# Kernel tuning notes

Hardware: AMD Instinct MI355X
Metric: run time of the kernel (lower is better)

## Reference

```python
import jax, jax.numpy as jnp
import numpy as np

N = 131072
C = 8
W = 256


def setup_inputs() -> dict:
    key = jax.random.key(0)
    ks = jax.random.split(key, 10)
    s1 = 1.0 / np.sqrt(3.0)
    sw = 1.0 / np.sqrt(W)
    return {
        "positions": jax.random.normal(ks[0], (N, 3), dtype=jnp.float32),
        "times": jax.random.randint(ks[1], (N,), 0, C, dtype=jnp.int64),
        "W1": jax.random.normal(ks[2], (C, 3, W), dtype=jnp.float32) * s1,
        "b1": jnp.zeros((C, W), dtype=jnp.float32),
        "W2": jax.random.normal(ks[3], (C, W, W), dtype=jnp.float32) * sw,
        "b2": jnp.zeros((C, W), dtype=jnp.float32),
        "W3": jax.random.normal(ks[4], (C, W, W), dtype=jnp.float32) * sw,
        "b3": jnp.zeros((C, W), dtype=jnp.float32),
        "W4": jax.random.normal(ks[5], (C, W, 3), dtype=jnp.float32) * sw,
        "b4": jnp.zeros((C, 3), dtype=jnp.float32),
    }


def _mlp(x, w1, c1, w2, c2, w3, c3, w4, c4):
    # 4-layer MLP, Tanh hidden activations and Tanh output activation
    h = jnp.tanh(x @ w1 + c1)
    h = jnp.tanh(h @ w2 + c2)
    h = jnp.tanh(h @ w3 + c3)
    return jnp.tanh(h @ w4 + c4)


def reference(positions, times, W1, b1, W2, b2, W3, b3, W4, b4):
    # offsets = zeros_like(positions); offsets[times==i] = mlp_i(positions[times==i])
    # classes partition the points, so this equals a per-class select-sum.
    offsets = jnp.zeros_like(positions)
    for i in range(C):  # small fixed class count
        out_i = _mlp(positions, W1[i], b1[i], W2[i], b2[i], W3[i], b3[i], W4[i], b4[i])
        mask = (times == i)[:, None]  # [N,1]
        offsets = jnp.where(mask, out_i, offsets)
    return offsets
```

## Files before the change

### kernel.cpp

```cpp
#include <hip/hip_runtime.h>
#include <stdint.h>

#define N_PTS 131072
#define NCLS 8
#define HID 256
#define MT 32
#define CAP 32768

#define PSC 2.8853900817779268f

typedef __bf16 bf16x8 __attribute__((ext_vector_type(8)));
typedef float f32x4 __attribute__((ext_vector_type(4)));

__device__ __forceinline__ float tanh_p2(float a) {
  return fmaf(-2.0f, __builtin_amdgcn_rcpf(__builtin_amdgcn_exp2f(a) + 1.0f), 1.0f);
}

__device__ __forceinline__ unsigned short f2bf_rne(float f) {
  unsigned u = __float_as_uint(f);
  u = u + 0x7fffu + ((u >> 16) & 1u);
  return (unsigned short)(u >> 16);
}

__device__ __forceinline__ unsigned pack_bf16(float a, float b) {
  unsigned ua = __float_as_uint(a) + 0x8000u;
  unsigned ub = __float_as_uint(b) + 0x8000u;
  return __builtin_amdgcn_perm(ub, ua, 0x07060302u);
}

#define PK_TILES 256
#define MISC_BLKS 177
#define MISC_N 45184
#define SCAT_BLKS 128
#define PREP_GRID (PK_TILES + MISC_BLKS + SCAT_BLKS)

__global__ __launch_bounds__(256) void k_prep(
    const int* __restrict__ times,
    const float* __restrict__ W1, const float* __restrict__ b1,
    const float* __restrict__ W2, const float* __restrict__ b2,
    const float* __restrict__ W3, const float* __restrict__ b3,
    const float* __restrict__ W4, const float* __restrict__ b4,
    int* __restrict__ hdr, int* __restrict__ sortedIdx,
    unsigned short* __restrict__ packed23,
    float* __restrict__ w1p, float* __restrict__ b2p,
    float* __restrict__ b3p, float* __restrict__ b4p,
    unsigned short* __restrict__ W4p) {
  __shared__ unsigned short T[64][64];

  int b = blockIdx.x;
  int tid = threadIdx.x;

  if (b < PK_TILES) {
    int cl = b >> 4;
    int l = cl >> 3, c = cl & 7;
    int tile = b & 15;
    int k0 = (tile >> 2) * 64, j0 = (tile & 3) * 64;
    const float* W = (l ? W3 : W2) + c * 65536;
#pragma unroll
    for (int it = 0; it < 4; it++) {
      int f = tid + it * 256;
      int row = f >> 4, cg = f & 15;
      float4 v = *(const float4*)&W[(k0 + row) * 256 + j0 + cg * 4];
      T[row][cg * 4 + 0] = f2bf_rne(PSC * v.x);
      T[row][cg * 4 + 1] = f2bf_rne(PSC * v.y);
      T[row][cg * 4 + 2] = f2bf_rne(PSC * v.z);
      T[row][cg * 4 + 3] = f2bf_rne(PSC * v.w);
    }
    __syncthreads();
#pragma unroll
    for (int it = 0; it < 2; it++) {
      int g = tid + it * 256;
      int kb = g >> 6, j = g & 63;
      unsigned u[8];
#pragma unroll
      for (int uu = 0; uu < 8; uu++) u[uu] = T[kb * 8 + uu][j];
      uint4 pk = make_uint4(u[0] | (u[1] << 16), u[2] | (u[3] << 16),
                            u[4] | (u[5] << 16), u[6] | (u[7] << 16));
      int base = cl * 65536 + (((k0 >> 3) + kb) * 256 + (j0 + j)) * 8;
      *(uint4*)&packed23[base] = pk;
    }
  } else if (b < PK_TILES + MISC_BLKS) {
    int e2 = (b - PK_TILES) * 256 + tid;
    if (e2 < 8192) {
      int c = e2 >> 10, rem = e2 & 1023;
      int j = rem >> 2, t = rem & 3;
      float v = (t < 3) ? W1[c * 768 + t * 256 + j] : b1[c * 256 + j];
      w1p[e2] = PSC * v;
    } else if (e2 < 10240) {
      int i = e2 - 8192;
      b2p[i] = PSC * b2[i];
    } else if (e2 < 12288) {
      int i = e2 - 10240;
      b3p[i] = PSC * b3[i];
    } else if (e2 < 12416) {
      int i = e2 - 12288;
      int c = i >> 4, r = i & 15;
      b4p[i] = (r < 3) ? PSC * b4[c * 3 + r] : 0.0f;
    } else if (e2 < MISC_N) {
      int i = e2 - 12416;
      int c = i >> 12, rem = i & 4095;
      int jj = rem & 7, j = (rem >> 3) & 15, k = ((rem >> 7) << 3) + jj;
      float v = (j < 3) ? PSC * W4[c * 768 + k * 3 + j] : 0.0f;
      W4p[c * 4096 + rem] = f2bf_rne(v);
    }
  } else {
    __shared__ int gcnt[16][NCLS];
    __shared__ int gpre[16][NCLS];
    __shared__ int gbase[NCLS];
    int sb = b - (PK_TILES + MISC_BLKS);
    int lane = tid & 63, w = tid >> 6;
    int4 tv = ((const int4*)times)[sb * 256 + tid];
    int tcl[4] = {tv.x, tv.y, tv.z, tv.w};
    int rank[4];
#pragma unroll
    for (int s = 0; s < 4; s++) {
      int t = tcl[s];
      unsigned long long m0 = __ballot(t == 0), m1 = __ballot(t == 1);
      unsigned long long m2 = __ballot(t == 2), m3 = __ballot(t == 3);
      unsigned long long m4 = __ballot(t == 4), m5 = __ballot(t == 5);
      unsigned long long m6 = __ballot(t == 6), m7 = __ballot(t == 7);
      unsigned long long x0 = (t & 1) ? m1 : m0, x1 = (t & 1) ? m3 : m2;
      unsigned long long x2 = (t & 1) ? m5 : m4, x3 = (t & 1) ? m7 : m6;
      unsigned long long y0 = (t & 2) ? x1 : x0, y1 = (t & 2) ? x3 : x2;
      unsigned long long mo = (t & 4) ? y1 : y0;
      rank[s] = __popcll(mo & ((1ull << lane) - 1ull));
      if (lane == 0) {
        int g = w * 4 + s;
        gcnt[g][0] = __popcll(m0); gcnt[g][1] = __popcll(m1);
        gcnt[g][2] = __popcll(m2); gcnt[g][3] = __popcll(m3);
        gcnt[g][4] = __popcll(m4); gcnt[g][5] = __popcll(m5);
        gcnt[g][6] = __popcll(m6); gcnt[g][7] = __popcll(m7);
      }
    }
    __syncthreads();
    if (tid < NCLS) {
      int run = 0;
#pragma unroll
      for (int g = 0; g < 16; g++) { gpre[g][tid] = run; run += gcnt[g][tid]; }
      gbase[tid] = run ? atomicAdd(&hdr[tid], run) : 0;
    }
    __syncthreads();
    int i0 = (sb * 256 + tid) * 4;
#pragma unroll
    for (int s = 0; s < 4; s++) {
      int t = tcl[s];
      int g = w * 4 + s;
      sortedIdx[t * CAP + gbase[t] + gpre[g][t] + rank[s]] = i0 + s;
    }
  }
}

__device__ __forceinline__ void mfma_layer_T(
    unsigned short (*__restrict__ Abuf)[MT][8],
    const unsigned short* __restrict__ Apack,
    const float* __restrict__ biasp,
    int tid) {
  int lane = tid & 63, w = tid >> 6;
  int quad = lane >> 4, l16 = lane & 15;
  int jcol = w * 32 + l16;
  const bf16x8* __restrict__ Af = (const bf16x8*)Apack;

  f32x4 acc[2][2];
#pragma unroll
  for (int jf = 0; jf < 2; jf++) {
    f32x4 bv = *(const f32x4*)&biasp[w * 32 + jf * 16 + quad * 4];
#pragma unroll
    for (int mt = 0; mt < 2; mt++) acc[jf][mt] = bv;
  }

  __builtin_amdgcn_s_setprio(1);
#pragma unroll
  for (int kb = 0; kb < 8; kb++) {
    int kq = kb * 4 + quad;
    bf16x8 af[2], bfr[2];
#pragma unroll
    for (int jf = 0; jf < 2; jf++) af[jf] = Af[kq * 256 + jcol + jf * 16];
#pragma unroll
    for (int mt = 0; mt < 2; mt++)
      bfr[mt] = *(const bf16x8*)&Abuf[kq][mt * 16 + l16][0];
#pragma unroll
    for (int jf = 0; jf < 2; jf++)
#pragma unroll
      for (int mt = 0; mt < 2; mt++)
        acc[jf][mt] = __builtin_amdgcn_mfma_f32_16x16x32_bf16(af[jf], bfr[mt], acc[jf][mt], 0, 0, 0);
  }
  __builtin_amdgcn_s_setprio(0);

  __syncthreads();

#pragma unroll
  for (int jf = 0; jf < 2; jf++) {
    int jbase = w * 32 + jf * 16 + quad * 4;
#pragma unroll
    for (int mt = 0; mt < 2; mt++) {
      float t0 = tanh_p2(acc[jf][mt][0]);
      float t1 = tanh_p2(acc[jf][mt][1]);
      float t2 = tanh_p2(acc[jf][mt][2]);
      float t3 = tanh_p2(acc[jf][mt][3]);
      uint2 pk = make_uint2(pack_bf16(t0, t1), pack_bf16(t2, t3));
      *(uint2*)&Abuf[jbase >> 3][mt * 16 + l16][jbase & 7] = pk;
    }
  }
}

__global__ __launch_bounds__(512, 8) void k_mlp(
    const float* __restrict__ pos,
    const int* __restrict__ hdr, const int* __restrict__ sortedIdx,
    const unsigned short* __restrict__ packed23,
    const float* __restrict__ w1p, const float* __restrict__ b2p,
    const float* __restrict__ b3p, const float* __restrict__ b4p,
    const unsigned short* __restrict__ W4p,
    float* __restrict__ out) {

  __shared__ __align__(16) unsigned short Abuf[32][MT][8];
  __shared__ __align__(16) float4 xpos4[MT];
  __shared__ int sIdx[MT];

  int b = blockIdx.x;
  int tid = threadIdx.x;

  int c = -1, t0 = 0, cnt = 0;
  {
    int ts = 0;
#pragma unroll
    for (int cc = 0; cc < NCLS; cc++) {
      int cc_cnt = hdr[cc];
      int tiles = (cc_cnt + MT - 1) >> 5;
      if (b >= ts && b < ts + tiles) { c = cc; t0 = b - ts; cnt = cc_cnt; }
      ts += tiles;
    }
  }
  if (c < 0) return;
  int base = c * CAP + t0 * MT;
  int mCount = min(MT, cnt - t0 * MT);

  if (tid < MT) sIdx[tid] = sortedIdx[base + min(tid, mCount - 1)];
  __syncthreads();
  if (tid < MT) {
    int idx = sIdx[tid] * 3;
    xpos4[tid] = make_float4(pos[idx], pos[idx + 1], pos[idx + 2], 0.0f);
  }
  __syncthreads();

  {
    const float4* __restrict__ w1g = (const float4*)(w1p + (size_t)c * 1024);
    int m = tid & (MT - 1), q = tid >> 5;
    float4 xp = xpos4[m];
#pragma unroll
    for (int i8 = 0; i8 < 2; i8++) {
      int j8 = q * 2 + i8;
      unsigned pk[4];
#pragma unroll
      for (int jp = 0; jp < 4; jp++) {
        float t[2];
#pragma unroll
        for (int u = 0; u < 2; u++) {
          float4 wv = w1g[j8 * 8 + jp * 2 + u];
          float a = fmaf(xp.x, wv.x, fmaf(xp.y, wv.y, fmaf(xp.z, wv.z, wv.w)));
          t[u] = tanh_p2(a);
        }
        pk[jp] = pack_bf16(t[0], t[1]);
      }
      *(uint4*)&Abuf[j8][m][0] = make_uint4(pk[0], pk[1], pk[2], pk[3]);
    }
  }
  __syncthreads();

  mfma_layer_T(Abuf, packed23 + ((size_t)c << 16), b2p + c * 256, tid);
  __syncthreads();
  mfma_layer_T(Abuf, packed23 + ((size_t)(8 + c) << 16), b3p + c * 256, tid);
  __syncthreads();

  {
    int lane = tid & 63, w = tid >> 6;
    if (w < 2) {
      int quad = lane >> 4, l16 = lane & 15;
      const bf16x8* __restrict__ W4f = (const bf16x8*)W4p;
      f32x4 acc = *(const f32x4*)&b4p[c * 16 + quad * 4];
      __builtin_amdgcn_s_setprio(1);
#pragma unroll
      for (int kb = 0; kb < 8; kb++) {
        int kq = kb * 4 + quad;
        bf16x8 a4 = W4f[(size_t)c * 512 + kq * 16 + l16];
        bf16x8 b4f = *(const bf16x8*)&Abuf[kq][w * 16 + l16][0];
        acc = __builtin_amdgcn_mfma_f32_16x16x32_bf16(a4, b4f, acc, 0, 0, 0);
      }
      __builtin_amdgcn_s_setprio(0);
      int m = w * 16 + l16;
      if (quad == 0 && m < mCount) {
        int o = sIdx[m] * 3;
        out[o + 0] = tanh_p2(acc[0]);
        out[o + 1] = tanh_p2(acc[1]);
        out[o + 2] = tanh_p2(acc[2]);
      }
    }
  }
}

extern "C" void kernel_launch(void* const* d_in, const int* in_sizes, int n_in,
                              void* d_out, int out_size, void* d_ws, size_t ws_size,
                              hipStream_t stream) {
  const float* pos = (const float*)d_in[0];
  const int* times = (const int*)d_in[1];
  const float* W1 = (const float*)d_in[2];
  const float* b1 = (const float*)d_in[3];
  const float* W2 = (const float*)d_in[4];
  const float* b2 = (const float*)d_in[5];
  const float* W3 = (const float*)d_in[6];
  const float* b3 = (const float*)d_in[7];
  const float* W4 = (const float*)d_in[8];
  const float* b4 = (const float*)d_in[9];

  char* ws = (char*)d_ws;
  int* hdr = (int*)ws;
  int* sortedIdx = (int*)(ws + 4096);
  float* w1p = (float*)(ws + 1052672);
  float* b2p = (float*)(ws + 1085440);
  float* b3p = (float*)(ws + 1093632);
  float* b4p = (float*)(ws + 1101824);
  unsigned short* W4p = (unsigned short*)(ws + 1102336);
  unsigned short* packed23 = (unsigned short*)(ws + (2u << 20));
  float* out = (float*)d_out;

  hipMemsetAsync(d_ws, 0, 64, stream);
  k_prep<<<PREP_GRID, 256, 0, stream>>>(times, W1, b1, W2, b2, W3, b3, W4, b4,
                                        hdr, sortedIdx, packed23,
                                        w1p, b2p, b3p, b4p, W4p);
  k_mlp<<<N_PTS / MT + NCLS, 512, 0, stream>>>(
      pos, hdr, sortedIdx, packed23, w1p, b2p, b3p, b4p, W4p, out);
}
```

Baseline: 143.2 us.

## Double point tile to 64 and switch hidden layers to 32x32x16 MFMA

Raises the per-block point tile from 32 to 64 so each weight fragment loaded from global memory feeds twice as many points. The hidden layers switch from 16x16x32 to 32x32x16 bf16 MFMA with two 16-element accumulators per wave. The first-layer weights are staged in shared memory, and launch bounds drop to 6 blocks per CU. In exchange the kernel uses more registers and LDS, runs half as many blocks, and pads more rows in each class's last tile.

```diff
diff --git a/kernel.cpp b/kernel.cpp
--- a/kernel.cpp
+++ b/kernel.cpp
@@ -4,13 +4,14 @@
 #define N_PTS 131072
 #define NCLS 8
 #define HID 256
-#define MT 32
+#define MT 64
 #define CAP 32768
 
 #define PSC 2.8853900817779268f
 
 typedef __bf16 bf16x8 __attribute__((ext_vector_type(8)));
 typedef float f32x4 __attribute__((ext_vector_type(4)));
+typedef float f32x16 __attribute__((ext_vector_type(16)));
 
 __device__ __forceinline__ float tanh_p2(float a) {
   return fmaf(-2.0f, __builtin_amdgcn_rcpf(__builtin_amdgcn_exp2f(a) + 1.0f), 1.0f);
@@ -150,60 +151,60 @@
   }
 }
 
-__device__ __forceinline__ void mfma_layer_T(
+__device__ __forceinline__ void epi32(
+    const f32x16& ac, unsigned short (*__restrict__ Abuf)[MT][8],
+    int rowbase, int m, int hi) {
+#pragma unroll
+  for (int a = 0; a < 4; a++) {
+    float t0 = tanh_p2(ac[4 * a + 0]);
+    float t1 = tanh_p2(ac[4 * a + 1]);
+    float t2 = tanh_p2(ac[4 * a + 2]);
+    float t3 = tanh_p2(ac[4 * a + 3]);
+    uint2 pk = make_uint2(pack_bf16(t0, t1), pack_bf16(t2, t3));
+    *(uint2*)&Abuf[rowbase + a][m][4 * hi] = pk;
+  }
+}
+
+__device__ __forceinline__ void mfma_layer_32(
     unsigned short (*__restrict__ Abuf)[MT][8],
     const unsigned short* __restrict__ Apack,
     const float* __restrict__ biasp,
     int tid) {
   int lane = tid & 63, w = tid >> 6;
-  int quad = lane >> 4, l16 = lane & 15;
-  int jcol = w * 32 + l16;
+  int hi = lane >> 5, l32 = lane & 31;
+  int jcol = w * 32 + l32;
   const bf16x8* __restrict__ Af = (const bf16x8*)Apack;
 
-  f32x4 acc[2][2];
-#pragma unroll
-  for (int jf = 0; jf < 2; jf++) {
-    f32x4 bv = *(const f32x4*)&biasp[w * 32 + jf * 16 + quad * 4];
-#pragma unroll
-    for (int mt = 0; mt < 2; mt++) acc[jf][mt] = bv;
+  f32x16 acc0, acc1;
+#pragma unroll
+  for (int a = 0; a < 4; a++) {
+    f32x4 bv = *(const f32x4*)&biasp[w * 32 + 8 * a + 4 * hi];
+#pragma unroll
+    for (int e = 0; e < 4; e++) {
+      acc0[4 * a + e] = bv[e];
+      acc1[4 * a + e] = bv[e];
+    }
   }
 
   __builtin_amdgcn_s_setprio(1);
 #pragma unroll
-  for (int kb = 0; kb < 8; kb++) {
-    int kq = kb * 4 + quad;
-    bf16x8 af[2], bfr[2];
-#pragma unroll
-    for (int jf = 0; jf < 2; jf++) af[jf] = Af[kq * 256 + jcol + jf * 16];
-#pragma unroll
-    for (int mt = 0; mt < 2; mt++)
-      bfr[mt] = *(const bf16x8*)&Abuf[kq][mt * 16 + l16][0];
-#pragma unroll
-    for (int jf = 0; jf < 2; jf++)
-#pragma unroll
-      for (int mt = 0; mt < 2; mt++)
-        acc[jf][mt] = __builtin_amdgcn_mfma_f32_16x16x32_bf16(af[jf], bfr[mt], acc[jf][mt], 0, 0, 0);
+  for (int ks = 0; ks < 16; ks++) {
+    int kq = ks * 2 + hi;
+    bf16x8 af = Af[kq * 256 + jcol];
+    bf16x8 b0 = *(const bf16x8*)&Abuf[kq][l32][0];
+    bf16x8 b1 = *(const bf16x8*)&Abuf[kq][32 + l32][0];
+    acc0 = __builtin_amdgcn_mfma_f32_32x32x16_bf16(af, b0, acc0, 0, 0, 0);
+    acc1 = __builtin_amdgcn_mfma_f32_32x32x16_bf16(af, b1, acc1, 0, 0, 0);
   }
   __builtin_amdgcn_s_setprio(0);
 
   __syncthreads();
 
-#pragma unroll
-  for (int jf = 0; jf < 2; jf++) {
-    int jbase = w * 32 + jf * 16 + quad * 4;
-#pragma unroll
-    for (int mt = 0; mt < 2; mt++) {
-      float t0 = tanh_p2(acc[jf][mt][0]);
-      float t1 = tanh_p2(acc[jf][mt][1]);
-      float t2 = tanh_p2(acc[jf][mt][2]);
-      float t3 = tanh_p2(acc[jf][mt][3]);
-      uint2 pk = make_uint2(pack_bf16(t0, t1), pack_bf16(t2, t3));
-      *(uint2*)&Abuf[jbase >> 3][mt * 16 + l16][jbase & 7] = pk;
-    }
-  }
-}
-
-__global__ __launch_bounds__(512, 8) void k_mlp(
+  epi32(acc0, Abuf, w * 4, l32, hi);
+  epi32(acc1, Abuf, w * 4, 32 + l32, hi);
+}
+
+__global__ __launch_bounds__(512, 6) void k_mlp(
     const float* __restrict__ pos,
     const int* __restrict__ hdr, const int* __restrict__ sortedIdx,
     const unsigned short* __restrict__ packed23,
@@ -213,6 +214,7 @@
     float* __restrict__ out) {
 
   __shared__ __align__(16) unsigned short Abuf[32][MT][8];
+  __shared__ __align__(16) float4 w1i[256];
   __shared__ __align__(16) float4 xpos4[MT];
   __shared__ int sIdx[MT];
 
@@ -225,7 +227,7 @@
 #pragma unroll
     for (int cc = 0; cc < NCLS; cc++) {
       int cc_cnt = hdr[cc];
-      int tiles = (cc_cnt + MT - 1) >> 5;
+      int tiles = (cc_cnt + MT - 1) >> 6;
       if (b >= ts && b < ts + tiles) { c = cc; t0 = b - ts; cnt = cc_cnt; }
       ts += tiles;
     }
@@ -235,6 +237,7 @@
   int mCount = min(MT, cnt - t0 * MT);
 
   if (tid < MT) sIdx[tid] = sortedIdx[base + min(tid, mCount - 1)];
+  if (tid < 256) w1i[tid] = ((const float4*)(w1p + (size_t)c * 1024))[tid];
   __syncthreads();
   if (tid < MT) {
     int idx = sIdx[tid] * 3;
@@ -243,19 +246,18 @@
   __syncthreads();
 
   {
-    const float4* __restrict__ w1g = (const float4*)(w1p + (size_t)c * 1024);
-    int m = tid & (MT - 1), q = tid >> 5;
+    int m = tid & 63, q = tid >> 6;
     float4 xp = xpos4[m];
 #pragma unroll
-    for (int i8 = 0; i8 < 2; i8++) {
-      int j8 = q * 2 + i8;
+    for (int i8 = 0; i8 < 4; i8++) {
+      int j8 = q * 4 + i8;
       unsigned pk[4];
 #pragma unroll
       for (int jp = 0; jp < 4; jp++) {
         float t[2];
 #pragma unroll
         for (int u = 0; u < 2; u++) {
-          float4 wv = w1g[j8 * 8 + jp * 2 + u];
+          float4 wv = w1i[j8 * 8 + jp * 2 + u];
           float a = fmaf(xp.x, wv.x, fmaf(xp.y, wv.y, fmaf(xp.z, wv.z, wv.w)));
           t[u] = tanh_p2(a);
         }
@@ -266,14 +268,14 @@
   }
   __syncthreads();
 
-  mfma_layer_T(Abuf, packed23 + ((size_t)c << 16), b2p + c * 256, tid);
-  __syncthreads();
-  mfma_layer_T(Abuf, packed23 + ((size_t)(8 + c) << 16), b3p + c * 256, tid);
+  mfma_layer_32(Abuf, packed23 + ((size_t)c << 16), b2p + c * 256, tid);
+  __syncthreads();
+  mfma_layer_32(Abuf, packed23 + ((size_t)(8 + c) << 16), b3p + c * 256, tid);
   __syncthreads();
 
   {
     int lane = tid & 63, w = tid >> 6;
-    if (w < 2) {
+    if (w < 4) {
       int quad = lane >> 4, l16 = lane & 15;
       const bf16x8* __restrict__ W4f = (const bf16x8*)W4p;
       f32x4 acc = *(const f32x4*)&b4p[c * 16 + quad * 4];
```

Result: faster. 134.7 us (-5.9%).
